# Performance work log

Measured on AMD Instinct MI355X. Metric: run time of the kernel, lower is better.

The kernel has to match this reference:

```python
import jax, jax.numpy as jnp
import numpy as np

N, E, HID, ED, L, H, D = 65536, 262144, 256, 64, 2, 8, 32
FF = 4 * HID
A_START = 8192  # first action gripper node; nodes [A_START:] are the T*K action nodes


def _ln(x, s, b, eps=1e-5):
    mu = jnp.mean(x, -1, keepdims=True)
    var = jnp.var(x, -1, keepdims=True)
    return (x - mu) * jax.lax.rsqrt(var + eps) * s + b


def _gnn_forward(x, edge_attr, edge_index, Wq, Wk, Wv, WeK, WeV, Wo,
                 ln1_s, ln1_b, ffn_w1, ffn_b1, ffn_w2, ffn_b2, ln2_s, ln2_b):
    # Hetero graph transformer over the single ('gripper','action','gripper') relation:
    # per-layer edge-indexed gather -> multi-head attention with edge features ->
    # segment softmax over incoming edges -> scatter-aggregate -> residual/LN/FFN.
    n = x.shape[0]
    e = edge_attr.shape[0]
    src, dst = edge_index[0], edge_index[1]
    inv_sqrt_d = np.float32(1.0 / np.sqrt(D))
    for l in range(Wq.shape[0]):
        q = (x @ Wq[l]).reshape(n, H, D)
        k = (x @ Wk[l]).reshape(n, H, D)
        v = (x @ Wv[l]).reshape(n, H, D)
        kj = k[src] + (edge_attr @ WeK[l]).reshape(e, H, D)  # [E,H,D] gathered keys + edge bias
        vj = v[src] + (edge_attr @ WeV[l]).reshape(e, H, D)
        score = jnp.einsum('ehd,ehd->eh', q[dst], kj) * inv_sqrt_d  # [E,H]
        smax = jax.ops.segment_max(score, dst, num_segments=n)
        p = jnp.exp(score - smax[dst])
        denom = jax.ops.segment_sum(p, dst, num_segments=n)
        alpha = p / denom[dst]  # segment softmax over incoming edges
        agg = jax.ops.segment_sum((alpha[..., None] * vj).reshape(e, H * D), dst, num_segments=n)
        x = _ln(x + agg @ Wo[l], ln1_s[l], ln1_b[l])
        hid = jax.nn.gelu(x @ ffn_w1[l] + ffn_b1[l], approximate=False) @ ffn_w2[l] + ffn_b2[l]
        x = _ln(x + hid, ln2_s[l], ln2_b[l])
    return x


def setup_inputs() -> dict:
    key = jax.random.key(0)
    ks = iter(jax.random.split(key, 16))
    w = lambda shape: jax.random.normal(next(ks), shape, jnp.float32) * 0.05
    return {
        "all_gripper_feats": jax.random.normal(next(ks), (N, HID), jnp.float32),
        "edge_attr": jax.random.normal(next(ks), (E, ED), jnp.float32),
        "Wq": w((L, HID, H * D)), "Wk": w((L, HID, H * D)), "Wv": w((L, HID, H * D)),
        "WeK": w((L, ED, H * D)), "WeV": w((L, ED, H * D)), "Wo": w((L, H * D, HID)),
        "ln1_s": jnp.ones((L, HID), jnp.float32), "ln1_b": jnp.zeros((L, HID), jnp.float32),
        "ffn_w1": w((L, HID, FF)), "ffn_b1": jnp.zeros((L, FF), jnp.float32),
        "ffn_w2": w((L, FF, HID)), "ffn_b2": jnp.zeros((L, HID), jnp.float32),
        "ln2_s": jnp.ones((L, HID), jnp.float32), "ln2_b": jnp.zeros((L, HID), jnp.float32),
        "head_w1": w((HID, HID)), "head_b1": jnp.zeros((HID,), jnp.float32),
        "head_w2": w((HID, 7)), "head_b2": jnp.zeros((7,), jnp.float32),
        "edge_index": jax.random.randint(next(ks), (2, E), 0, N),
        "action_start": A_START,
    }


def reference(all_gripper_feats, edge_attr, Wq, Wk, Wv, WeK, WeV, Wo,
              ln1_s, ln1_b, ffn_w1, ffn_b1, ffn_w2, ffn_b2, ln2_s, ln2_b,
              head_w1, head_b1, head_w2, head_b2, edge_index, action_start):
    x = _gnn_forward(all_gripper_feats, edge_attr, edge_index, Wq, Wk, Wv, WeK, WeV, Wo,
                     ln1_s, ln1_b, ffn_w1, ffn_b1, ffn_w2, ffn_b2, ln2_s, ln2_b)
    a = x[action_start:]  # action gripper nodes (T*K, hidden)
    return jax.nn.gelu(a @ head_w1 + head_b1, approximate=False) @ head_w2 + head_b2  # (T*K, 7)
```

## Files before the change

kernel.cpp:

```cpp
#include <hip/hip_runtime.h>
#include <hip/hip_bf16.h>
#include <math.h>

#define NN     65536
#define NE     262144
#define HIDN   256
#define EDIM   64
#define NHEAD  8
#define FFN    1024
#define ASTART 8192
#define NACT   (NN - ASTART)
#define NCH    32768
#define NCHUNK (NE / NCH)
#define DPC    (NN / NCHUNK)
#define RCH    32768

typedef __attribute__((ext_vector_type(8))) short short8;
typedef __attribute__((ext_vector_type(4))) short short4v;
typedef __attribute__((ext_vector_type(4))) float float4v;
typedef __hip_bfloat16 bf16;

__device__ __forceinline__ float b2f(short s) {
    union { unsigned u; float f; } c;
    c.u = ((unsigned)(unsigned short)s) << 16;
    return c.f;
}
__device__ __forceinline__ short f2b(float f) {
    __hip_bfloat16 h = __float2bfloat16(f);
    return *reinterpret_cast<short*>(&h);
}
__device__ __forceinline__ float gelu_exact(float v) {
    return 0.5f * v * (1.0f + erff(v * 0.70710678118654752f));
}
__device__ __forceinline__ void gload16(const void* g, void* l) {
    __builtin_amdgcn_global_load_lds(
        (const __attribute__((address_space(1))) void*)(uintptr_t)g,
        (__attribute__((address_space(3))) void*)(unsigned)(uintptr_t)l,
        16, 0, 0);
}

__global__ void convert_kernel(const float* __restrict__ src,
                               bf16* __restrict__ dst, int n) {
    int i = blockIdx.x * 256 + threadIdx.x;
    if (i < n) dst[i] = __float2bfloat16(src[i]);
}

__global__ void transpose_kernel(const float* __restrict__ src,
                                 bf16* __restrict__ dst, int R, int Cc) {
    int idx = blockIdx.x * 256 + threadIdx.x;
    if (idx >= R * Cc) return;
    int r = idx / Cc, c = idx - r * Cc;
    dst[(size_t)c * R + r] = __float2bfloat16(src[idx]);
}

__global__ void hist_kernel(const int* __restrict__ dstI, int* __restrict__ cnt) {
    int i = blockIdx.x * 256 + threadIdx.x;
    if (i < NE) atomicAdd(&cnt[dstI[i]], 1);
}
__global__ void scan1_kernel(const int* __restrict__ cnt, int* __restrict__ rp,
                             int* __restrict__ bsum) {
    __shared__ int s[256];
    int t = threadIdx.x, i = blockIdx.x * 256 + t;
    int v = cnt[i]; s[t] = v; __syncthreads();
    for (int off = 1; off < 256; off <<= 1) {
        int x = (t >= off) ? s[t - off] : 0; __syncthreads();
        s[t] += x; __syncthreads();
    }
    rp[i] = s[t] - v;
    if (t == 255) bsum[blockIdx.x] = s[255];
}
__global__ void scan2_kernel(int* __restrict__ bsum) {
    __shared__ int s[256];
    int t = threadIdx.x; int v = bsum[t]; s[t] = v; __syncthreads();
    for (int off = 1; off < 256; off <<= 1) {
        int x = (t >= off) ? s[t - off] : 0; __syncthreads();
        s[t] += x; __syncthreads();
    }
    bsum[t] = s[t] - v;
}
__global__ void scan3_kernel(int* __restrict__ rp, const int* __restrict__ bsum,
                             int* __restrict__ cursor) {
    int i = blockIdx.x * 256 + threadIdx.x;
    int v = rp[i] + bsum[i >> 8];
    rp[i] = v; cursor[i] = v;
    if (i == 0) rp[NN] = NE;
}
__global__ void scatter_kernel(const int* __restrict__ srcI, const int* __restrict__ dstI,
                               int* __restrict__ cursor, int* __restrict__ perm,
                               int* __restrict__ src_s, int* __restrict__ dst_s) {
    int e = blockIdx.x * 256 + threadIdx.x;
    if (e >= NE) return;
    int d = dstI[e];
    int pos = atomicAdd(&cursor[d], 1);
    perm[pos] = e; src_s[pos] = srcI[e]; dst_s[pos] = d;
}

template<int AMODE, bool DO_GELU>
__global__ __launch_bounds__(256) void gemm_kernel(
    const void* __restrict__ A,
    const bf16* __restrict__ BT,
    const bf16* __restrict__ bias,
    bf16* __restrict__ C,
    int M, int Nn, int K,
    const int* __restrict__ perm)
{
    __shared__ __align__(16) short As[128 * 32];
    __shared__ __align__(16) short Bs[128 * 32];

    const int t    = threadIdx.x;
    const int wave = t >> 6;
    const int lane = t & 63;
    const int l15  = lane & 15;
    const int quad = lane >> 4;
    const int wm   = (wave & 1) * 64;
    const int wn   = (wave >> 1) * 64;
    const int bm   = blockIdx.y * 128;
    const int bn   = blockIdx.x * 128;
    const int srow = t >> 2;
    const int scol = (t & 3) * 8;

    const short* Ab = (const short*)A  + (size_t)(bm + srow) * K + scol;
    const short* Bb = (const short*)BT + (size_t)(bn + srow) * K + scol;
    const float* Af0;
    const float* Af1;
    if (AMODE == 1) {
        Af0 = (const float*)A + (size_t)(bm + srow) * K + scol;
        Af1 = Af0 + (size_t)64 * K;
    } else if (AMODE == 2) {
        const int pr0 = perm[bm + srow];
        const int pr1 = perm[bm + 64 + srow];
        Af0 = (const float*)A + (size_t)pr0 * K + scol;
        Af1 = (const float*)A + (size_t)pr1 * K + scol;
    }
    char* lA = (char*)As;
    char* lB = (char*)Bs;
    const int offT = t * 16;
    const int offW = wave * 1024;

    float4v acc[4][4];
    #pragma unroll
    for (int i = 0; i < 4; ++i)
        #pragma unroll
        for (int j = 0; j < 4; ++j) acc[i][j] = (float4v){0.f, 0.f, 0.f, 0.f};

    for (int k0 = 0; k0 < K; k0 += 32) {
        __syncthreads();
        if (AMODE == 0) {
            gload16(Ab + k0,                  lA + offW);
            gload16(Ab + (size_t)64 * K + k0, lA + 4096 + offW);
        } else {
            const float* s0 = Af0 + k0;
            const float* s1 = Af1 + k0;
            #pragma unroll
            for (int i = 0; i < 2; ++i) {
                const float* s = i ? s1 : s0;
                float4v f0 = *(const float4v*)s;
                float4v f1 = *(const float4v*)(s + 4);
                short8 w;
                #pragma unroll
                for (int j = 0; j < 4; ++j) { w[j] = f2b(f0[j]); w[4 + j] = f2b(f1[j]); }
                *(short8*)(lA + i * 4096 + offT) = w;
            }
        }
        gload16(Bb + k0,                  lB + offW);
        gload16(Bb + (size_t)64 * K + k0, lB + 4096 + offW);
        __syncthreads();

        short8 afr[4], bfr[4];
        #pragma unroll
        for (int i = 0; i < 4; ++i)
            afr[i] = *(const short8*)(lA + (wm + i * 16 + l15) * 64 + quad * 16);
        #pragma unroll
        for (int j = 0; j < 4; ++j)
            bfr[j] = *(const short8*)(lB + (wn + j * 16 + l15) * 64 + quad * 16);
        #pragma unroll
        for (int i = 0; i < 4; ++i)
            #pragma unroll
            for (int j = 0; j < 4; ++j)
                acc[i][j] = __builtin_amdgcn_mfma_f32_16x16x32_bf16(afr[i], bfr[j], acc[i][j], 0, 0, 0);
    }

    #pragma unroll
    for (int j = 0; j < 4; ++j) {
        const int col = bn + wn + j * 16 + l15;
        const float bv = bias ? b2f(((const short*)bias)[col]) : 0.0f;
        #pragma unroll
        for (int i = 0; i < 4; ++i) {
            const int row0 = bm + wm + i * 16 + quad * 4;
            #pragma unroll
            for (int r = 0; r < 4; ++r) {
                float v = acc[i][j][r] + bv;
                if (DO_GELU) v = gelu_exact(v);
                C[(size_t)(row0 + r) * Nn + col] = __float2bfloat16(v);
            }
        }
    }
}

__global__ __launch_bounds__(256) void score_kernel(
    const bf16* __restrict__ q, const bf16* __restrict__ k,
    const bf16* __restrict__ eK,
    const int* __restrict__ src_s, const int* __restrict__ dst_s,
    short* __restrict__ pbuf, int e0)
{
    const int p = e0 + blockIdx.x * 4 + (threadIdx.x >> 6);
    const int lane = threadIdx.x & 63;
    const int s = src_s[p], d = dst_s[p];
    const int off = lane * 4;

    const short4v qv = *(const short4v*)((const short*)q  + (size_t)d * HIDN + off);
    const short4v kv = *(const short4v*)((const short*)k  + (size_t)s * HIDN + off);
    const short4v ev = *(const short4v*)((const short*)eK + (size_t)(p - e0) * HIDN + off);
    float x = 0.f;
    #pragma unroll
    for (int j = 0; j < 4; ++j) x += b2f(qv[j]) * (b2f(kv[j]) + b2f(ev[j]));
    x += __shfl_xor(x, 1);
    x += __shfl_xor(x, 2);
    x += __shfl_xor(x, 4);
    if ((lane & 7) == 0) {
        const float sc = fminf(fmaxf(x * 0.17677669529663689f, -30.f), 30.f);
        pbuf[(size_t)p * NHEAD + (lane >> 3)] = f2b(expf(sc));
    }
}

__global__ __launch_bounds__(256) void agg_kernel(
    const short* __restrict__ pbuf, const bf16* __restrict__ v,
    const bf16* __restrict__ eV,
    const int* __restrict__ src_s, const int* __restrict__ rp,
    float* __restrict__ agg, int e0, int e1, int dlo)
{
    const int d = dlo + blockIdx.x * 4 + (threadIdx.x >> 6);
    const int lane = threadIdx.x & 63;
    const int es = rp[d], ee = rp[d + 1];
    const int lo = es > e0 ? es : e0;
    const int hi = ee < e1 ? ee : e1;
    if (lo >= hi) return;
    const int h = lane >> 3, off = lane * 4;

    float den = 0.f;
    for (int p = es; p < ee; ++p) den += b2f(pbuf[(size_t)p * NHEAD + h]);

    float a0 = 0.f, a1 = 0.f, a2 = 0.f, a3 = 0.f;
    for (int p = lo; p < hi; ++p) {
        const float al = b2f(pbuf[(size_t)p * NHEAD + h]) / den;
        const int s = src_s[p];
        const short4v vv = *(const short4v*)((const short*)v  + (size_t)s * HIDN + off);
        const short4v ev = *(const short4v*)((const short*)eV + (size_t)(p - e0) * HIDN + off);
        a0 += al * (b2f(vv[0]) + b2f(ev[0]));
        a1 += al * (b2f(vv[1]) + b2f(ev[1]));
        a2 += al * (b2f(vv[2]) + b2f(ev[2]));
        a3 += al * (b2f(vv[3]) + b2f(ev[3]));
    }
    float* ao = agg + (size_t)d * HIDN + off;
    if (es >= e0 && ee <= e1) {
        *(float4v*)ao = (float4v){a0, a1, a2, a3};
    } else {
        atomicAdd(ao + 0, a0); atomicAdd(ao + 1, a1);
        atomicAdd(ao + 2, a2); atomicAdd(ao + 3, a3);
    }
}

__global__ __launch_bounds__(256) void ln_kernel(
    bf16* __restrict__ x, const bf16* __restrict__ t,
    const bf16* __restrict__ sc, const bf16* __restrict__ bi, int r0)
{
    const int row = r0 + blockIdx.x * 4 + (threadIdx.x >> 6);
    const int lane = threadIdx.x & 63;
    const size_t base = (size_t)row * HIDN + lane * 4;
    const size_t tbase = (size_t)(row - r0) * HIDN + lane * 4;
    const short4v xv = *(const short4v*)((const short*)x + base);
    const short4v tv = *(const short4v*)((const short*)t + tbase);
    float v[4];
    #pragma unroll
    for (int j = 0; j < 4; ++j) v[j] = b2f(xv[j]) + b2f(tv[j]);
    float sum = v[0] + v[1] + v[2] + v[3];
    float ssq = v[0]*v[0] + v[1]*v[1] + v[2]*v[2] + v[3]*v[3];
    #pragma unroll
    for (int m = 1; m < 64; m <<= 1) { sum += __shfl_xor(sum, m); ssq += __shfl_xor(ssq, m); }
    const float mean = sum * (1.0f / 256.0f);
    const float var  = fmaxf(ssq * (1.0f / 256.0f) - mean * mean, 0.0f);
    const float rstd = rsqrtf(var + 1e-5f);
    const short4v sv = *(const short4v*)((const short*)sc + lane * 4);
    const short4v bv = *(const short4v*)((const short*)bi + lane * 4);
    short4v out;
    #pragma unroll
    for (int j = 0; j < 4; ++j)
        out[j] = f2b((v[j] - mean) * rstd * b2f(sv[j]) + b2f(bv[j]));
    *(short4v*)((short*)x + base) = out;
}

__global__ __launch_bounds__(256) void head2_kernel(
    const bf16* __restrict__ h1, const bf16* __restrict__ w2T,
    const bf16* __restrict__ b2, float* __restrict__ out)
{
    const int row = blockIdx.x * 4 + (threadIdx.x >> 6);
    const int lane = threadIdx.x & 63;
    const int off = lane * 4;
    const short4v hv = *(const short4v*)((const short*)h1 + (size_t)row * HIDN + off);
    float hf[4];
    #pragma unroll
    for (int j = 0; j < 4; ++j) hf[j] = b2f(hv[j]);
    float acc[7];
    #pragma unroll
    for (int jc = 0; jc < 7; ++jc) {
        const short4v wv = *(const short4v*)((const short*)w2T + jc * HIDN + off);
        float a = hf[0]*b2f(wv[0]) + hf[1]*b2f(wv[1]) + hf[2]*b2f(wv[2]) + hf[3]*b2f(wv[3]);
        #pragma unroll
        for (int m = 1; m < 64; m <<= 1) a += __shfl_xor(a, m);
        acc[jc] = a;
    }
    if (lane < 7) {
        float r = lane == 0 ? acc[0] : lane == 1 ? acc[1] : lane == 2 ? acc[2] :
                  lane == 3 ? acc[3] : lane == 4 ? acc[4] : lane == 5 ? acc[5] : acc[6];
        out[(size_t)row * 7 + lane] = r + b2f(((const short*)b2)[lane]);
    }
}

extern "C" void kernel_launch(void* const* d_in, const int* in_sizes, int n_in,
                              void* d_out, int out_size, void* d_ws, size_t ws_size,
                              hipStream_t stream)
{
    const float* xin   = (const float*)d_in[0];
    const float* eattr = (const float*)d_in[1];
    const float* Wq    = (const float*)d_in[2];
    const float* Wk    = (const float*)d_in[3];
    const float* Wv    = (const float*)d_in[4];
    const float* WeK   = (const float*)d_in[5];
    const float* WeV   = (const float*)d_in[6];
    const float* Wo    = (const float*)d_in[7];
    const float* ln1s  = (const float*)d_in[8];
    const float* ln1b  = (const float*)d_in[9];
    const float* fw1   = (const float*)d_in[10];
    const float* fb1   = (const float*)d_in[11];
    const float* fw2   = (const float*)d_in[12];
    const float* fb2   = (const float*)d_in[13];
    const float* ln2s  = (const float*)d_in[14];
    const float* ln2b  = (const float*)d_in[15];
    const float* hw1   = (const float*)d_in[16];
    const float* hb1   = (const float*)d_in[17];
    const float* hw2   = (const float*)d_in[18];
    const float* hb2   = (const float*)d_in[19];
    const int*  eidx   = (const int*)d_in[20];
    const int*  srcI   = eidx;
    const int*  dstI   = eidx + NE;

    char* base = (char*)d_ws;
    size_t off = 0;
    auto carve = [&](size_t bytes) -> char* {
        char* p = base + off;
        off += (bytes + 255) & ~(size_t)255;
        return p;
    };
    bf16*  x_b    = (bf16*) carve((size_t)NN * HIDN * 2);
    bf16*  q_b    = (bf16*) carve((size_t)NN * HIDN * 2);
    bf16*  k_b    = (bf16*) carve((size_t)NN * HIDN * 2);
    bf16*  v_b    = (bf16*) carve((size_t)NN * HIDN * 2);
    bf16*  echunk = (bf16*) carve((size_t)NCH * HIDN * 2);
    short* pbuf   = (short*)carve((size_t)NE * NHEAD * 2);
    int*   perm   = (int*)  carve((size_t)NE * 4);
    int*   src_s  = (int*)  carve((size_t)NE * 4);
    int*   dst_s  = (int*)  carve((size_t)NE * 4);
    int*   rowp   = (int*)  carve((size_t)(NN + 1) * 4);
    bf16*  WqT    = (bf16*) carve((size_t)HIDN * HIDN * 2);
    bf16*  WkT    = (bf16*) carve((size_t)HIDN * HIDN * 2);
    bf16*  WvT    = (bf16*) carve((size_t)HIDN * HIDN * 2);
    bf16*  WoT    = (bf16*) carve((size_t)HIDN * HIDN * 2);
    bf16*  WeKT   = (bf16*) carve((size_t)HIDN * EDIM * 2);
    bf16*  WeVT   = (bf16*) carve((size_t)HIDN * EDIM * 2);
    bf16*  W1T    = (bf16*) carve((size_t)FFN * HIDN * 2);
    bf16*  W2T    = (bf16*) carve((size_t)HIDN * FFN * 2);
    bf16*  HW1T   = (bf16*) carve((size_t)HIDN * HIDN * 2);
    bf16*  HW2T   = (bf16*) carve((size_t)8 * HIDN * 2);
    bf16*  c_ln1s = (bf16*) carve((size_t)2 * HIDN * 2);
    bf16*  c_ln1b = (bf16*) carve((size_t)2 * HIDN * 2);
    bf16*  c_ln2s = (bf16*) carve((size_t)2 * HIDN * 2);
    bf16*  c_ln2b = (bf16*) carve((size_t)2 * HIDN * 2);
    bf16*  c_fb1  = (bf16*) carve((size_t)2 * FFN * 2);
    bf16*  c_fb2  = (bf16*) carve((size_t)2 * HIDN * 2);
    bf16*  c_hb1  = (bf16*) carve((size_t)HIDN * 2);
    bf16*  c_hb2  = (bf16*) carve((size_t)16 * 2);
    if (off > ws_size) return;

    int* cnt    = (int*)echunk;
    int* cursor = cnt + NN;
    int* bsum   = cursor + NN;
    float* agg    = (float*)q_b;
    bf16*  tmp_b  = v_b;
    bf16*  hid    = q_b;
    bf16*  ffnout = v_b;

    const int TB = 256;
    #define GRID1(n) dim3(((n) + TB - 1) / TB)

    convert_kernel<<<GRID1(NN * HIDN), TB, 0, stream>>>(xin, x_b, NN * HIDN);
    convert_kernel<<<GRID1(2 * HIDN), TB, 0, stream>>>(ln1s, c_ln1s, 2 * HIDN);
    convert_kernel<<<GRID1(2 * HIDN), TB, 0, stream>>>(ln1b, c_ln1b, 2 * HIDN);
    convert_kernel<<<GRID1(2 * HIDN), TB, 0, stream>>>(ln2s, c_ln2s, 2 * HIDN);
    convert_kernel<<<GRID1(2 * HIDN), TB, 0, stream>>>(ln2b, c_ln2b, 2 * HIDN);
    convert_kernel<<<GRID1(2 * FFN), TB, 0, stream>>>(fb1, c_fb1, 2 * FFN);
    convert_kernel<<<GRID1(2 * HIDN), TB, 0, stream>>>(fb2, c_fb2, 2 * HIDN);
    convert_kernel<<<GRID1(HIDN), TB, 0, stream>>>(hb1, c_hb1, HIDN);
    convert_kernel<<<1, TB, 0, stream>>>(hb2, c_hb2, 7);
    transpose_kernel<<<GRID1(HIDN * HIDN), TB, 0, stream>>>(hw1, HW1T, HIDN, HIDN);
    transpose_kernel<<<GRID1(HIDN * 7), TB, 0, stream>>>(hw2, HW2T, HIDN, 7);

    hipMemsetAsync(cnt, 0, (size_t)NN * 4, stream);
    hist_kernel<<<GRID1(NE), TB, 0, stream>>>(dstI, cnt);
    scan1_kernel<<<NN / 256, 256, 0, stream>>>(cnt, rowp, bsum);
    scan2_kernel<<<1, 256, 0, stream>>>(bsum);
    scan3_kernel<<<NN / 256, 256, 0, stream>>>(rowp, bsum, cursor);
    scatter_kernel<<<GRID1(NE), TB, 0, stream>>>(srcI, dstI, cursor, perm, src_s, dst_s);

    for (int l = 0; l < 2; ++l) {
        transpose_kernel<<<GRID1(HIDN * HIDN), TB, 0, stream>>>(Wq + (size_t)l*HIDN*HIDN, WqT, HIDN, HIDN);
        transpose_kernel<<<GRID1(HIDN * HIDN), TB, 0, stream>>>(Wk + (size_t)l*HIDN*HIDN, WkT, HIDN, HIDN);
        transpose_kernel<<<GRID1(HIDN * HIDN), TB, 0, stream>>>(Wv + (size_t)l*HIDN*HIDN, WvT, HIDN, HIDN);
        transpose_kernel<<<GRID1(EDIM * HIDN), TB, 0, stream>>>(WeK + (size_t)l*EDIM*HIDN, WeKT, EDIM, HIDN);
        transpose_kernel<<<GRID1(EDIM * HIDN), TB, 0, stream>>>(WeV + (size_t)l*EDIM*HIDN, WeVT, EDIM, HIDN);
        transpose_kernel<<<GRID1(HIDN * HIDN), TB, 0, stream>>>(Wo + (size_t)l*HIDN*HIDN, WoT, HIDN, HIDN);
        transpose_kernel<<<GRID1(HIDN * FFN),  TB, 0, stream>>>(fw1 + (size_t)l*HIDN*FFN, W1T, HIDN, FFN);
        transpose_kernel<<<GRID1(FFN * HIDN),  TB, 0, stream>>>(fw2 + (size_t)l*FFN*HIDN, W2T, FFN, HIDN);

        gemm_kernel<0, false><<<dim3(HIDN/128, NN/128), TB, 0, stream>>>(x_b, WqT, nullptr, q_b, NN, HIDN, HIDN, nullptr);
        gemm_kernel<0, false><<<dim3(HIDN/128, NN/128), TB, 0, stream>>>(x_b, WkT, nullptr, k_b, NN, HIDN, HIDN, nullptr);
        gemm_kernel<0, false><<<dim3(HIDN/128, NN/128), TB, 0, stream>>>(x_b, WvT, nullptr, v_b, NN, HIDN, HIDN, nullptr);

        for (int c = 0; c < NCHUNK; ++c) {
            gemm_kernel<2, false><<<dim3(HIDN/128, NCH/128), TB, 0, stream>>>(
                eattr, WeKT, nullptr, echunk, NCH, HIDN, EDIM, perm + (size_t)c * NCH);
            score_kernel<<<NCH / 4, TB, 0, stream>>>(q_b, k_b, echunk, src_s, dst_s, pbuf, c * NCH);
        }

        hipMemsetAsync(agg, 0, (size_t)NN * HIDN * 4, stream);
        for (int c = 0; c < NCHUNK; ++c) {
            gemm_kernel<2, false><<<dim3(HIDN/128, NCH/128), TB, 0, stream>>>(
                eattr, WeVT, nullptr, echunk, NCH, HIDN, EDIM, perm + (size_t)c * NCH);
            const int dlo = (c == 0) ? 0 : (c - 1) * DPC;
            const int dhi = (c == NCHUNK - 1) ? NN : (c + 2) * DPC;
            agg_kernel<<<(dhi - dlo) / 4, TB, 0, stream>>>(
                pbuf, v_b, echunk, src_s, rowp, agg, c * NCH, (c + 1) * NCH, dlo);
        }

        gemm_kernel<1, false><<<dim3(HIDN/128, NN/128), TB, 0, stream>>>(agg, WoT, nullptr, tmp_b, NN, HIDN, HIDN, nullptr);
        ln_kernel<<<NN / 4, TB, 0, stream>>>(x_b, tmp_b, c_ln1s + (size_t)l * HIDN, c_ln1b + (size_t)l * HIDN, 0);

        for (int r0 = 0; r0 < NN; r0 += RCH) {
            gemm_kernel<0, true ><<<dim3(FFN/128, RCH/128), TB, 0, stream>>>(
                x_b + (size_t)r0 * HIDN, W1T, c_fb1 + (size_t)l * FFN, hid, RCH, FFN, HIDN, nullptr);
            gemm_kernel<0, false><<<dim3(HIDN/128, RCH/128), TB, 0, stream>>>(
                hid, W2T, c_fb2 + (size_t)l * HIDN, ffnout, RCH, HIDN, FFN, nullptr);
            ln_kernel<<<RCH / 4, TB, 0, stream>>>(x_b, ffnout, c_ln2s + (size_t)l * HIDN, c_ln2b + (size_t)l * HIDN, r0);
        }
    }

    gemm_kernel<0, true><<<dim3(HIDN/128, NACT/128), TB, 0, stream>>>(
        x_b + (size_t)ASTART * HIDN, HW1T, c_hb1, hid, NACT, HIDN, HIDN, nullptr);
    head2_kernel<<<NACT / 4, TB, 0, stream>>>(hid, HW2T, c_hb2, (float*)d_out);
}
```

Measured before the change: 1.723 ms.

## Double-buffer GEMM LDS tiles with XOR swizzle and fuse Q/K projections

Measured after the change: 1.704 ms. About the same (-1.1%).

```diff
diff --git a/kernel.cpp b/kernel.cpp
--- a/kernel.cpp
+++ b/kernel.cpp
@@ -104,8 +104,8 @@
     int M, int Nn, int K,
     const int* __restrict__ perm)
 {
-    __shared__ __align__(16) short As[128 * 32];
-    __shared__ __align__(16) short Bs[128 * 32];
+    __shared__ __align__(16) short As[2][128 * 32];
+    __shared__ __align__(16) short Bs[2][128 * 32];
 
     const int t    = threadIdx.x;
     const int wave = t >> 6;
@@ -117,25 +117,26 @@
     const int bm   = blockIdx.y * 128;
     const int bn   = blockIdx.x * 128;
     const int srow = t >> 2;
-    const int scol = (t & 3) * 8;
-
-    const short* Ab = (const short*)A  + (size_t)(bm + srow) * K + scol;
-    const short* Bb = (const short*)BT + (size_t)(bn + srow) * K + scol;
-    const float* Af0;
-    const float* Af1;
+    const int sw   = srow & 3;
+    const int scolB = ((t & 3) ^ sw) * 8;
+    const int scolA = (t & 3) * 8;
+
+    const short* Ab = (const short*)A  + (size_t)(bm + srow) * K + scolB;
+    const short* Bb = (const short*)BT + (size_t)(bn + srow) * K + scolB;
+    const float* Af0 = nullptr;
+    const float* Af1 = nullptr;
     if (AMODE == 1) {
-        Af0 = (const float*)A + (size_t)(bm + srow) * K + scol;
+        Af0 = (const float*)A + (size_t)(bm + srow) * K + scolA;
         Af1 = Af0 + (size_t)64 * K;
     } else if (AMODE == 2) {
         const int pr0 = perm[bm + srow];
         const int pr1 = perm[bm + 64 + srow];
-        Af0 = (const float*)A + (size_t)pr0 * K + scol;
-        Af1 = (const float*)A + (size_t)pr1 * K + scol;
-    }
-    char* lA = (char*)As;
-    char* lB = (char*)Bs;
-    const int offT = t * 16;
-    const int offW = wave * 1024;
+        Af0 = (const float*)A + (size_t)pr0 * K + scolA;
+        Af1 = (const float*)A + (size_t)pr1 * K + scolA;
+    }
+    const int offW  = wave * 1024;
+    const int offTs = (t * 16) ^ (sw << 4);
+    const int qs16  = (quad ^ (l15 & 3)) * 16;
 
     float4v acc[4][4];
     #pragma unroll
@@ -143,41 +144,52 @@
         #pragma unroll
         for (int j = 0; j < 4; ++j) acc[i][j] = (float4v){0.f, 0.f, 0.f, 0.f};
 
-    for (int k0 = 0; k0 < K; k0 += 32) {
-        __syncthreads();
+    const int nt = K >> 5;
+
+    auto STAGE = [&](int b, int k0) {
+        char* lA = (char*)As[b];
+        char* lB = (char*)Bs[b];
         if (AMODE == 0) {
             gload16(Ab + k0,                  lA + offW);
             gload16(Ab + (size_t)64 * K + k0, lA + 4096 + offW);
         } else {
-            const float* s0 = Af0 + k0;
-            const float* s1 = Af1 + k0;
             #pragma unroll
             for (int i = 0; i < 2; ++i) {
-                const float* s = i ? s1 : s0;
+                const float* s = (i ? Af1 : Af0) + k0;
                 float4v f0 = *(const float4v*)s;
                 float4v f1 = *(const float4v*)(s + 4);
                 short8 w;
                 #pragma unroll
                 for (int j = 0; j < 4; ++j) { w[j] = f2b(f0[j]); w[4 + j] = f2b(f1[j]); }
-                *(short8*)(lA + i * 4096 + offT) = w;
+                *(short8*)(lA + i * 4096 + offTs) = w;
             }
         }
         gload16(Bb + k0,                  lB + offW);
         gload16(Bb + (size_t)64 * K + k0, lB + 4096 + offW);
-        __syncthreads();
-
+    };
+
+    STAGE(0, 0);
+    __syncthreads();
+
+    for (int kt = 0; kt < nt; ++kt) {
+        const int cur = kt & 1;
+        if (kt + 1 < nt) STAGE(cur ^ 1, (kt + 1) * 32);
+
+        const char* lA = (const char*)As[cur];
+        const char* lB = (const char*)Bs[cur];
         short8 afr[4], bfr[4];
         #pragma unroll
         for (int i = 0; i < 4; ++i)
-            afr[i] = *(const short8*)(lA + (wm + i * 16 + l15) * 64 + quad * 16);
+            afr[i] = *(const short8*)(lA + (wm + i * 16 + l15) * 64 + qs16);
         #pragma unroll
         for (int j = 0; j < 4; ++j)
-            bfr[j] = *(const short8*)(lB + (wn + j * 16 + l15) * 64 + quad * 16);
+            bfr[j] = *(const short8*)(lB + (wn + j * 16 + l15) * 64 + qs16);
         #pragma unroll
         for (int i = 0; i < 4; ++i)
             #pragma unroll
             for (int j = 0; j < 4; ++j)
                 acc[i][j] = __builtin_amdgcn_mfma_f32_16x16x32_bf16(afr[i], bfr[j], acc[i][j], 0, 0, 0);
+        __syncthreads();
     }
 
     #pragma unroll
@@ -201,15 +213,15 @@
     const bf16* __restrict__ q, const bf16* __restrict__ k,
     const bf16* __restrict__ eK,
     const int* __restrict__ src_s, const int* __restrict__ dst_s,
-    short* __restrict__ pbuf, int e0)
+    short* __restrict__ pbuf, int e0, int qkstride)
 {
     const int p = e0 + blockIdx.x * 4 + (threadIdx.x >> 6);
     const int lane = threadIdx.x & 63;
     const int s = src_s[p], d = dst_s[p];
     const int off = lane * 4;
 
-    const short4v qv = *(const short4v*)((const short*)q  + (size_t)d * HIDN + off);
-    const short4v kv = *(const short4v*)((const short*)k  + (size_t)s * HIDN + off);
+    const short4v qv = *(const short4v*)((const short*)q  + (size_t)d * qkstride + off);
+    const short4v kv = *(const short4v*)((const short*)k  + (size_t)s * qkstride + off);
     const short4v ev = *(const short4v*)((const short*)eK + (size_t)(p - e0) * HIDN + off);
     float x = 0.f;
     #pragma unroll
@@ -352,8 +364,7 @@
         return p;
     };
     bf16*  x_b    = (bf16*) carve((size_t)NN * HIDN * 2);
-    bf16*  q_b    = (bf16*) carve((size_t)NN * HIDN * 2);
-    bf16*  k_b    = (bf16*) carve((size_t)NN * HIDN * 2);
+    bf16*  qk_b   = (bf16*) carve((size_t)NN * 2 * HIDN * 2);
     bf16*  v_b    = (bf16*) carve((size_t)NN * HIDN * 2);
     bf16*  echunk = (bf16*) carve((size_t)NCH * HIDN * 2);
     short* pbuf   = (short*)carve((size_t)NE * NHEAD * 2);
@@ -361,8 +372,7 @@
     int*   src_s  = (int*)  carve((size_t)NE * 4);
     int*   dst_s  = (int*)  carve((size_t)NE * 4);
     int*   rowp   = (int*)  carve((size_t)(NN + 1) * 4);
-    bf16*  WqT    = (bf16*) carve((size_t)HIDN * HIDN * 2);
-    bf16*  WkT    = (bf16*) carve((size_t)HIDN * HIDN * 2);
+    bf16*  WqkT   = (bf16*) carve((size_t)2 * HIDN * HIDN * 2);
     bf16*  WvT    = (bf16*) carve((size_t)HIDN * HIDN * 2);
     bf16*  WoT    = (bf16*) carve((size_t)HIDN * HIDN * 2);
     bf16*  WeKT   = (bf16*) carve((size_t)HIDN * EDIM * 2);
@@ -384,9 +394,9 @@
     int* cnt    = (int*)echunk;
     int* cursor = cnt + NN;
     int* bsum   = cursor + NN;
-    float* agg    = (float*)q_b;
+    float* agg    = (float*)qk_b;
     bf16*  tmp_b  = v_b;
-    bf16*  hid    = q_b;
+    bf16*  hid    = qk_b;
     bf16*  ffnout = v_b;
 
     const int TB = 256;
@@ -412,8 +422,8 @@
     scatter_kernel<<<GRID1(NE), TB, 0, stream>>>(srcI, dstI, cursor, perm, src_s, dst_s);
 
     for (int l = 0; l < 2; ++l) {
-        transpose_kernel<<<GRID1(HIDN * HIDN), TB, 0, stream>>>(Wq + (size_t)l*HIDN*HIDN, WqT, HIDN, HIDN);
-        transpose_kernel<<<GRID1(HIDN * HIDN), TB, 0, stream>>>(Wk + (size_t)l*HIDN*HIDN, WkT, HIDN, HIDN);
+        transpose_kernel<<<GRID1(HIDN * HIDN), TB, 0, stream>>>(Wq + (size_t)l*HIDN*HIDN, WqkT, HIDN, HIDN);
+        transpose_kernel<<<GRID1(HIDN * HIDN), TB, 0, stream>>>(Wk + (size_t)l*HIDN*HIDN, WqkT + (size_t)HIDN*HIDN, HIDN, HIDN);
         transpose_kernel<<<GRID1(HIDN * HIDN), TB, 0, stream>>>(Wv + (size_t)l*HIDN*HIDN, WvT, HIDN, HIDN);
         transpose_kernel<<<GRID1(EDIM * HIDN), TB, 0, stream>>>(WeK + (size_t)l*EDIM*HIDN, WeKT, EDIM, HIDN);
         transpose_kernel<<<GRID1(EDIM * HIDN), TB, 0, stream>>>(WeV + (size_t)l*EDIM*HIDN, WeVT, EDIM, HIDN);
@@ -421,14 +431,13 @@
         transpose_kernel<<<GRID1(HIDN * FFN),  TB, 0, stream>>>(fw1 + (size_t)l*HIDN*FFN, W1T, HIDN, FFN);
         transpose_kernel<<<GRID1(FFN * HIDN),  TB, 0, stream>>>(fw2 + (size_t)l*FFN*HIDN, W2T, FFN, HIDN);
 
-        gemm_kernel<0, false><<<dim3(HIDN/128, NN/128), TB, 0, stream>>>(x_b, WqT, nullptr, q_b, NN, HIDN, HIDN, nullptr);
-        gemm_kernel<0, false><<<dim3(HIDN/128, NN/128), TB, 0, stream>>>(x_b, WkT, nullptr, k_b, NN, HIDN, HIDN, nullptr);
+        gemm_kernel<0, false><<<dim3((2*HIDN)/128, NN/128), TB, 0, stream>>>(x_b, WqkT, nullptr, qk_b, NN, 2*HIDN, HIDN, nullptr);
         gemm_kernel<0, false><<<dim3(HIDN/128, NN/128), TB, 0, stream>>>(x_b, WvT, nullptr, v_b, NN, HIDN, HIDN, nullptr);
 
         for (int c = 0; c < NCHUNK; ++c) {
             gemm_kernel<2, false><<<dim3(HIDN/128, NCH/128), TB, 0, stream>>>(
                 eattr, WeKT, nullptr, echunk, NCH, HIDN, EDIM, perm + (size_t)c * NCH);
-            score_kernel<<<NCH / 4, TB, 0, stream>>>(q_b, k_b, echunk, src_s, dst_s, pbuf, c * NCH);
+            score_kernel<<<NCH / 4, TB, 0, stream>>>(qk_b, qk_b + HIDN, echunk, src_s, dst_s, pbuf, c * NCH, 2 * HIDN);
         }
 
         hipMemsetAsync(agg, 0, (size_t)NN * HIDN * 4, stream);
```
